# Optimization experiments

Hardware: AMD Instinct MI355X
Metric: run time of the kernel (lower is better)

The kernel has to match this reference:

```python
import jax, jax.numpy as jnp
import numpy as np

T, HID, H, KV, D = 2048, 2048, 16, 8, 128
EPS = 1e-6
THETA = 10000.0


def setup_inputs() -> dict:
    key = jax.random.key(0)
    ks = jax.random.split(key, 4)
    return {
        "positions": jnp.arange(T, dtype=jnp.int32),
        "hidden_states": jax.random.normal(ks[0], (T, HID), dtype=jnp.float32),
        "layernorm_weight": jnp.ones((HID,), dtype=jnp.float32),
        "qkv_weight": jax.random.normal(ks[1], ((H + 2 * KV) * D, HID), dtype=jnp.float32) * 0.02,
        "q_norm_weight": jnp.ones((D,), dtype=jnp.float32),
        "k_norm_weight": jnp.ones((D,), dtype=jnp.float32),
        "o_weight": jax.random.normal(ks[2], (HID, H * D), dtype=jnp.float32) * 0.02,
    }


def _rms(x, w, eps=EPS):
    var = jnp.mean(jnp.square(x), axis=-1, keepdims=True)
    return x * jax.lax.rsqrt(var + eps) * w


def _rope(x, pos):
    # NeoX-style rotary over full head_dim. x: [T, nH, D]
    inv_freq = 1.0 / (THETA ** (jnp.arange(0, D, 2, dtype=jnp.float32) / D))
    ang = pos.astype(jnp.float32)[:, None] * inv_freq  # [T, D/2]
    cos, sin = jnp.cos(ang)[:, None, :], jnp.sin(ang)[:, None, :]
    x1, x2 = x[..., : D // 2], x[..., D // 2 :]
    return jnp.concatenate([x1 * cos - x2 * sin, x2 * cos + x1 * sin], axis=-1)


def reference(positions, hidden_states, layernorm_weight, qkv_weight,
              q_norm_weight, k_norm_weight, o_weight):
    # Fused RMSNorm + QKV projection
    normed = _rms(hidden_states, layernorm_weight)                 # [T, HID]
    qkv = normed @ qkv_weight.T                                    # [T, (H+2KV)*D]
    q, k, v = jnp.split(qkv, [H * D, (H + KV) * D], axis=-1)
    q = _rms(q.reshape(T, H, D), q_norm_weight)                    # per-head q norm
    k = _rms(k.reshape(T, KV, D), k_norm_weight)                   # per-head k norm
    v = v.reshape(T, KV, D)
    # RoPE
    q = _rope(q, positions)
    k = _rope(k, positions)
    # GQA causal attention
    scale = D ** -0.5
    kr = jnp.repeat(k, H // KV, axis=1)                            # [T, H, D]
    vr = jnp.repeat(v, H // KV, axis=1)
    scores = jnp.einsum("qhd,khd->hqk", q, kr) * scale             # [H, T, T]
    mask = jnp.tril(jnp.ones((T, T), dtype=bool))
    scores = jnp.where(mask[None], scores, jnp.finfo(scores.dtype).min)
    attn = jax.nn.softmax(scores, axis=-1)
    out = jnp.einsum("hqk,khd->qhd", attn, vr).reshape(T, H * D)
    return out @ o_weight.T                                        # [T, HID]
```

## Files before the change

### kernel.cpp

```cpp
#include <hip/hip_runtime.h>
#include <cstdint>
#include <cstddef>

typedef __bf16 bf16;
typedef __attribute__((ext_vector_type(8))) __bf16 bf16x8;
typedef __attribute__((ext_vector_type(4))) __bf16 bf16x4v;
typedef __attribute__((ext_vector_type(4))) float f32x4;
typedef __attribute__((ext_vector_type(16))) float f32x16;
typedef __attribute__((ext_vector_type(4))) short short4v;

#define T_N   2048
#define HID_N 2048
#define NH    16
#define NKV   8
#define HD    128

#define MFMA(a, b, c)   __builtin_amdgcn_mfma_f32_16x16x32_bf16((a), (b), (c), 0, 0, 0)
#define MFMA32(a, b, c) __builtin_amdgcn_mfma_f32_32x32x16_bf16((a), (b), (c), 0, 0, 0)

__device__ __forceinline__ f32x4 MFMA16(short4v a, short4v b, f32x4 c) {
#if __has_builtin(__builtin_amdgcn_mfma_f32_16x16x16bf16_1k)
    return __builtin_amdgcn_mfma_f32_16x16x16bf16_1k(a, b, c, 0, 0, 0);
#else
    asm volatile("v_mfma_f32_16x16x16_bf16 %0, %1, %2, %0\n\ts_nop 7\n\ts_nop 7"
                 : "+v"(c) : "v"(a), "v"(b));
    return c;
#endif
}

__device__ __forceinline__ void gl_lds16(const void* g, void* l) {
    __builtin_amdgcn_global_load_lds(
        (const __attribute__((address_space(1))) unsigned int*)g,
        (__attribute__((address_space(3))) unsigned int*)l,
        16, 0, 0);
}

__device__ __forceinline__ uint32_t pk2(float a, float b) {
    union { bf16 h; unsigned short u; } ca, cb;
    ca.h = (bf16)a; cb.h = (bf16)b;
    return ((uint32_t)cb.u << 16) | ca.u;
}

__device__ __forceinline__ void y2cq(int y, int& ci, int& qt) {
    if (y < 25)       { ci = 0; qt = y + 7; }
    else if (y < 42)  { ci = 1; qt = y - 10; }
    else if (y < 51)  { ci = 2; qt = y - 19; }
    else if (y == 51) { ci = 3; qt = 31; }
    else { int z = y - 52; int k = 7 - (z >> 2); ci = z & 3; qt = 8 * ci + k - 1; }
}
__device__ __forceinline__ int yof(int ci, int qt) {
    int k = qt + 1 - 8 * ci;
    if (k >= 8) {
        if (ci == 0) return qt - 7;
        if (ci == 1) return qt + 10;
        if (ci == 2) return qt + 19;
        return 51;
    }
    return 52 + (7 - k) * 4 + ci;
}

__global__ __launch_bounds__(256) void k_pre(const float* __restrict__ qkvw,
                                             bf16* __restrict__ qkvw_b,
                                             const float* __restrict__ ow,
                                             bf16* __restrict__ ow_b,
                                             const float* __restrict__ hid,
                                             const float* __restrict__ lw,
                                             bf16* __restrict__ normed) {
    const int blk = blockIdx.x, tid = threadIdx.x;
    if (blk < 6144) {
        const float* src; bf16* dst;
        if (blk < 4096) { int i = blk * 2048 + tid * 8; src = qkvw + i; dst = qkvw_b + i; }
        else            { int i = (blk - 4096) * 2048 + tid * 8; src = ow + i; dst = ow_b + i; }
        float4 x = ((const float4*)src)[0], y = ((const float4*)src)[1];
        bf16x8 v;
        v[0] = (bf16)x.x; v[1] = (bf16)x.y; v[2] = (bf16)x.z; v[3] = (bf16)x.w;
        v[4] = (bf16)y.x; v[5] = (bf16)y.y; v[6] = (bf16)y.z; v[7] = (bf16)y.w;
        *(bf16x8*)dst = v;
        return;
    }
    const int row = blk - 6144;
    const float* xr = hid + (size_t)row * HID_N;
    float4 a = ((const float4*)xr)[tid * 2];
    float4 b = ((const float4*)xr)[tid * 2 + 1];
    float ss = a.x*a.x + a.y*a.y + a.z*a.z + a.w*a.w
             + b.x*b.x + b.y*b.y + b.z*b.z + b.w*b.w;
    #pragma unroll
    for (int m = 32; m; m >>= 1) ss += __shfl_xor(ss, m);
    __shared__ float red[4];
    if ((tid & 63) == 0) red[tid >> 6] = ss;
    __syncthreads();
    float tot = red[0] + red[1] + red[2] + red[3];
    float rs = rsqrtf(tot * (1.0f / HID_N) + 1e-6f);
    const float4* wr = (const float4*)(lw + tid * 8);
    float4 wa = wr[0], wb = wr[1];
    bf16x8 v;
    v[0] = (bf16)(a.x * rs * wa.x); v[1] = (bf16)(a.y * rs * wa.y);
    v[2] = (bf16)(a.z * rs * wa.z); v[3] = (bf16)(a.w * rs * wa.w);
    v[4] = (bf16)(b.x * rs * wb.x); v[5] = (bf16)(b.y * rs * wb.y);
    v[6] = (bf16)(b.z * rs * wb.z); v[7] = (bf16)(b.w * rs * wb.w);
    *(bf16x8*)(normed + (size_t)row * HID_N + tid * 8) = v;
}

__global__ __launch_bounds__(256, 3) void k_gemm_qkv(const bf16* __restrict__ A,
                                                     const bf16* __restrict__ B,
                                                     bf16* __restrict__ qkv3,
                                                     bf16* __restrict__ vb) {
    const int K = HID_N;
    __shared__ __attribute__((aligned(16))) bf16 As[128 * 64];
    __shared__ __attribute__((aligned(16))) bf16 Bs[128 * 64];
    const int tid = threadIdx.x;
    const int lane = tid & 63, wid = tid >> 6;
    const int wm = wid >> 1, wn = wid & 1;
    const int col31 = lane & 31, khalf = lane >> 5;
    const int orig = blockIdx.y * gridDim.x + blockIdx.x;
    const int wgid = (orig & 7) * 64 + (orig >> 3);
    const size_t bm = (size_t)(wgid >> 5) * 128, bn = (size_t)(wgid & 31) * 128;

    f32x16 acc[2][2] = {};
    const int srow = tid >> 3;
    const int schk = tid & 7;

    for (int k0 = 0; k0 < K; k0 += 64) {
        __syncthreads();
        #pragma unroll
        for (int c = 0; c < 4; c++) {
            int row = c * 32 + srow;
            int ka = (schk ^ (row & 7)) << 3;
            gl_lds16(A + (bm + row) * (size_t)K + k0 + ka,
                     (char*)As + c * 4096 + tid * 16);
            gl_lds16(B + (bn + row) * (size_t)K + k0 + ka,
                     (char*)Bs + c * 4096 + tid * 16);
        }
        __syncthreads();
        #pragma unroll
        for (int kb = 0; kb < 4; kb++) {
            bf16x8 af[2], bfr[2];
            #pragma unroll
            for (int mt = 0; mt < 2; mt++) {
                int row = wm * 64 + mt * 32 + col31;
                af[mt] = *(const bf16x8*)(As + row * 64 + (((2 * kb + khalf) ^ (row & 7)) << 3));
            }
            #pragma unroll
            for (int nt = 0; nt < 2; nt++) {
                int row = wn * 64 + nt * 32 + col31;
                bfr[nt] = *(const bf16x8*)(Bs + row * 64 + (((2 * kb + khalf) ^ (row & 7)) << 3));
            }
            #pragma unroll
            for (int mt = 0; mt < 2; mt++)
                #pragma unroll
                for (int nt = 0; nt < 2; nt++)
                    acc[mt][nt] = MFMA32(af[mt], bfr[nt], acc[mt][nt]);
        }
    }
    #pragma unroll
    for (int mt = 0; mt < 2; mt++)
        #pragma unroll
        for (int nt = 0; nt < 2; nt++)
            #pragma unroll
            for (int i = 0; i < 16; i++) {
                int rowl = (i & 3) + 8 * (i >> 2) + 4 * khalf;
                size_t row = bm + wm * 64 + mt * 32 + rowl;
                size_t col = bn + wn * 64 + nt * 32 + col31;
                bf16 val = (bf16)acc[mt][nt][i];
                if (col < 3072) qkv3[row * 3072 + col] = val;
                else            vb[row * 1024 + (col - 3072)] = val;
            }
}

__global__ __launch_bounds__(256, 3) void k_gemm_bt64(const bf16* __restrict__ A,
                                                      const bf16* __restrict__ B,
                                                      float* __restrict__ C,
                                                      int M, int N, int K) {
    __shared__ __attribute__((aligned(16))) bf16 As[64 * 64];
    __shared__ __attribute__((aligned(16))) bf16 Bs[128 * 64];
    const int tid = threadIdx.x;
    const int lane = tid & 63, wid = tid >> 6;
    const int col31 = lane & 31, khalf = lane >> 5;
    const int orig = blockIdx.y * gridDim.x + blockIdx.x;
    const int wgid = (orig & 7) * 64 + (orig >> 3);
    const size_t bm = (size_t)(wgid >> 4) * 64, bn = (size_t)(wgid & 15) * 128;

    f32x16 acc[2] = {};
    const int srow = tid >> 3;
    const int schk = tid & 7;

    for (int k0 = 0; k0 < K; k0 += 64) {
        __syncthreads();
        #pragma unroll
        for (int c = 0; c < 2; c++) {
            int row = c * 32 + srow;
            int ka = (schk ^ (row & 7)) << 3;
            gl_lds16(A + (bm + row) * (size_t)K + k0 + ka,
                     (char*)As + c * 4096 + tid * 16);
        }
        #pragma unroll
        for (int c = 0; c < 4; c++) {
            int row = c * 32 + srow;
            int ka = (schk ^ (row & 7)) << 3;
            gl_lds16(B + (bn + row) * (size_t)K + k0 + ka,
                     (char*)Bs + c * 4096 + tid * 16);
        }
        __syncthreads();
        #pragma unroll
        for (int kb = 0; kb < 4; kb++) {
            bf16x8 af[2], bfr;
            #pragma unroll
            for (int mt = 0; mt < 2; mt++) {
                int row = mt * 32 + col31;
                af[mt] = *(const bf16x8*)(As + row * 64 + (((2 * kb + khalf) ^ (row & 7)) << 3));
            }
            {
                int row = wid * 32 + col31;
                bfr = *(const bf16x8*)(Bs + row * 64 + (((2 * kb + khalf) ^ (row & 7)) << 3));
            }
            #pragma unroll
            for (int mt = 0; mt < 2; mt++)
                acc[mt] = MFMA32(af[mt], bfr, acc[mt]);
        }
    }
    #pragma unroll
    for (int mt = 0; mt < 2; mt++)
        #pragma unroll
        for (int i = 0; i < 16; i++) {
            int rowl = (i & 3) + 8 * (i >> 2) + 4 * khalf;
            size_t row = bm + mt * 32 + rowl;
            size_t col = bn + wid * 32 + col31;
            C[row * (size_t)N + col] = acc[mt][i];
        }
}

__global__ __launch_bounds__(256) void k_mid(const bf16* __restrict__ qkv3,
                                             const float* __restrict__ qw,
                                             const float* __restrict__ kw,
                                             const int* __restrict__ pos,
                                             bf16* __restrict__ q,
                                             bf16* __restrict__ k,
                                             const bf16* __restrict__ vin,
                                             bf16* __restrict__ vT) {
    const int tid = threadIdx.x;
    if (blockIdx.y == 12) {
        const int bx = blockIdx.x;
        if (bx >= 512) return;
        __shared__ bf16 tile[64][72];
        const int tb = bx & 31, db = bx >> 5;
        const int row = tid >> 2, cc = tid & 3;
        const bf16* src = vin + (size_t)(tb * 64 + row) * 1024 + db * 64 + cc * 16;
        bf16x8 a = *(const bf16x8*)(src);
        bf16x8 b = *(const bf16x8*)(src + 8);
        #pragma unroll
        for (int i = 0; i < 8; i++) tile[row][cc * 16 + i] = a[i];
        #pragma unroll
        for (int i = 0; i < 8; i++) tile[row][cc * 16 + 8 + i] = b[i];
        __syncthreads();
        bf16* dst = vT + (size_t)(db * 64 + row) * 2048 + tb * 64 + cc * 16;
        bf16x8 o1, o2;
        #pragma unroll
        for (int i = 0; i < 8; i++) o1[i] = tile[cc * 16 + i][row];
        #pragma unroll
        for (int i = 0; i < 8; i++) o2[i] = tile[cc * 16 + 8 + i][row];
        *(bf16x8*)dst = o1;
        *(bf16x8*)(dst + 8) = o2;
        return;
    }
    const int t = blockIdx.x;
    const int half = tid >> 7, d = tid & 127;
    const int slot = blockIdx.y * 2 + half;
    const bool isq = slot < 16;
    const int h = isq ? slot : slot - 16;
    float x = (float)qkv3[(size_t)t * 3072 + slot * 128 + d];
    float ss = x * x;
    #pragma unroll
    for (int m = 32; m; m >>= 1) ss += __shfl_xor(ss, m);
    __shared__ float red[4];
    __shared__ float sh[256];
    if ((tid & 63) == 0) red[tid >> 6] = ss;
    __syncthreads();
    float rs = rsqrtf((red[half * 2] + red[half * 2 + 1]) * (1.0f / HD) + 1e-6f);
    float nx = x * rs * (isq ? qw[d] : kw[d]);
    sh[tid] = nx;
    __syncthreads();
    float other = sh[tid ^ 64];
    int j = d & 63;
    float ang = (float)pos[t] * __powf(10000.f, -(float)j * (1.f / 64.f));
    float s, c;
    __sincosf(ang, &s, &c);
    float o = (d < 64) ? (nx * c - other * s) : (nx * c + other * s);
    bf16* dst = isq ? (q + ((size_t)t * NH + h) * HD + d)
                    : (k + ((size_t)t * NKV + h) * HD + d);
    *dst = (bf16)o;
}

__global__ __launch_bounds__(256, 3) void k_flash(const bf16* __restrict__ Q,
                                                  const bf16* __restrict__ K,
                                                  const bf16* __restrict__ VT,
                                                  bf16* __restrict__ On,
                                                  float* __restrict__ ml) {
    __shared__ __attribute__((aligned(16))) bf16 Ks2[2][64 * 128];
    __shared__ __attribute__((aligned(16))) bf16 Vt[128 * 64];

    const int tid = threadIdx.x, lane = tid & 63, w = tid >> 6;
    const int r = lane & 15, g = lane >> 4;
    const int h = blockIdx.x, y = blockIdx.y;
    int ci, qt;
    y2cq(y, ci, qt);
    const int c0 = ci * 8;
    const int ntl = min(qt + 1 - c0, 8);
    const int q0 = qt * 64;
    const int gh = h >> 1;
    const int q0w = q0 + w * 16;

    const int rowk = tid >> 4, posc = tid & 15;
    const int vrow = tid >> 3, vkb = tid & 7;
    const bf16* VTh = VT + (size_t)gh * 128 * 2048;

    bf16x8 qf[4];
    #pragma unroll
    for (int ks = 0; ks < 4; ks++)
        qf[ks] = *(const bf16x8*)(Q + ((size_t)(q0w + r) * NH + h) * HD + ks * 32 + g * 8);

    f32x4 acc[8] = {};
    float m_run = -1e30f, l_run = 0.f;
    const float scale = 0.08838834764831845f;

    {
        const int kv0 = c0 * 64;
        #pragma unroll
        for (int c = 0; c < 4; c++) {
            int row = c * 16 + rowk;
            int srcc = posc ^ (row & 7);
            gl_lds16(K + ((size_t)(kv0 + row) * NKV + gh) * HD + srcc * 8,
                     (char*)&Ks2[0][0] + c * 4096 + tid * 16);
        }
        asm volatile("s_waitcnt vmcnt(0)" ::: "memory");
        __builtin_amdgcn_s_barrier();
    }

    for (int t = 0; t < ntl; ++t) {
        const int b = t & 1;
        const int kv0 = (c0 + t) * 64;
        const bool pf = (t + 1 < ntl);
        #pragma unroll
        for (int it = 0; it < 4; it++) {
            int d = it * 32 + vrow;
            int srck = (vkb ^ (vrow & 7)) * 8;
            gl_lds16(VTh + (size_t)d * 2048 + kv0 + srck,
                     (char*)&Vt[0] + it * 4096 + tid * 16);
        }
        if (pf) {
            const int kv1 = kv0 + 64;
            #pragma unroll
            for (int c = 0; c < 4; c++) {
                int row = c * 16 + rowk;
                int srcc = posc ^ (row & 7);
                gl_lds16(K + ((size_t)(kv1 + row) * NKV + gh) * HD + srcc * 8,
                         (char*)&Ks2[0][0] + (b ^ 1) * 16384 + c * 4096 + tid * 16);
            }
        }
        const bool compute = (kv0 <= q0w + 15);
        union PB { uint32_t u[2]; short4v s; };
        PB pbu[4];
        if (compute) {
            const bf16* Kb = &Ks2[b][0];
            const bool fullt = (kv0 + 63 <= q0w);
            float sc[4][4];
            __builtin_amdgcn_s_setprio(1);
            #pragma unroll
            for (int t4 = 0; t4 < 4; t4++) {
                f32x4 S = {};
                #pragma unroll
                for (int ks = 0; ks < 4; ks++) {
                    int row = t4 * 16 + r;
                    bf16x8 kf = *(const bf16x8*)(Kb + row * 128 + (((4 * ks + g) ^ (row & 7)) * 8));
                    S = MFMA(kf, qf[ks], S);
                }
                if (fullt) {
                    #pragma unroll
                    for (int j = 0; j < 4; j++) sc[t4][j] = S[j] * scale;
                } else {
                    #pragma unroll
                    for (int j = 0; j < 4; j++) {
                        int kg = kv0 + t4 * 16 + 4 * g + j;
                        sc[t4][j] = (kg <= q0w + r) ? S[j] * scale : -1e30f;
                    }
                }
            }
            __builtin_amdgcn_s_setprio(0);
            float mx = sc[0][0];
            #pragma unroll
            for (int t4 = 0; t4 < 4; t4++)
                #pragma unroll
                for (int j = 0; j < 4; j++) mx = fmaxf(mx, sc[t4][j]);
            mx = fmaxf(mx, __shfl_xor(mx, 16));
            mx = fmaxf(mx, __shfl_xor(mx, 32));
            const bool nr = __all(mx <= m_run + 8.0f) != 0;
            float mn, alpha;
            if (nr) { mn = m_run; alpha = 1.0f; }
            else    { mn = fmaxf(m_run, mx); alpha = __expf(m_run - mn); m_run = mn; }
            float rsum = 0.f;
            #pragma unroll
            for (int t4 = 0; t4 < 4; t4++)
                #pragma unroll
                for (int j = 0; j < 4; j++) {
                    sc[t4][j] = __expf(sc[t4][j] - mn);
                    rsum += sc[t4][j];
                }
            rsum += __shfl_xor(rsum, 16);
            rsum += __shfl_xor(rsum, 32);
            l_run = l_run * alpha + rsum;
            if (!nr) {
                #pragma unroll
                for (int f = 0; f < 8; f++)
                    #pragma unroll
                    for (int j = 0; j < 4; j++) acc[f][j] *= alpha;
            }
            #pragma unroll
            for (int t4 = 0; t4 < 4; t4++) {
                pbu[t4].u[0] = pk2(sc[t4][0], sc[t4][1]);
                pbu[t4].u[1] = pk2(sc[t4][2], sc[t4][3]);
            }
        }
        if (pf) asm volatile("s_waitcnt vmcnt(4)" ::: "memory");
        else    asm volatile("s_waitcnt vmcnt(0)" ::: "memory");
        __builtin_amdgcn_s_barrier();
        if (compute) {
            const char* Vb = (const char*)&Vt[0];
            __builtin_amdgcn_s_setprio(1);
            #pragma unroll
            for (int f = 0; f < 8; f++) {
                #pragma unroll
                for (int t4 = 0; t4 < 4; t4++) {
                    short4v vf = *(const short4v*)(Vb + f * 2048 + r * 128 +
                                  (((2 * t4 + (g >> 1)) ^ (r & 7)) * 16) + (g & 1) * 8);
                    acc[f] = MFMA16(vf, pbu[t4].s, acc[f]);
                }
            }
            __builtin_amdgcn_s_setprio(0);
        }
        asm volatile("s_waitcnt vmcnt(0)" ::: "memory");
        __builtin_amdgcn_s_barrier();
    }
    const int lr = w * 16 + r;
    float inv_l = 1.0f / l_run;
    bf16* Ob = On + ((size_t)(h * 80 + y)) * 8192 + lr * 128;
    #pragma unroll
    for (int f = 0; f < 8; f++) {
        bf16x4v ov;
        #pragma unroll
        for (int j = 0; j < 4; j++) ov[j] = (bf16)(acc[f][j] * inv_l);
        *(bf16x4v*)(Ob + f * 16 + 4 * g) = ov;
    }
    if (g == 0) {
        float* mlp = ml + ((size_t)(h * 80 + y)) * 128;
        mlp[lr] = m_run;
        mlp[64 + lr] = l_run;
    }
}

__global__ __launch_bounds__(256) void k_comb(const bf16* __restrict__ On,
                                              const float* __restrict__ ml,
                                              bf16* __restrict__ ao) {
    const int h = blockIdx.x, qt = blockIdx.y;
    const int tid = threadIdx.x;
    const int dc = tid & 15;
    const int qr = tid >> 4;
    const int nc = 1 + (qt >= 8) + (qt >= 16) + (qt >= 24);
    int ys[4];
    #pragma unroll
    for (int i = 0; i < 4; i++) ys[i] = (i < nc) ? yof(i, qt) : 0;
    #pragma unroll
    for (int p = 0; p < 4; p++) {
        const int lq = p * 16 + qr;
        float mi[4], li[4], wi[4];
        float mstar = -1e30f;
        for (int i = 0; i < 4; i++) {
            if (i < nc) {
                const float* pml = ml + ((size_t)(h * 80 + ys[i])) * 128;
                mi[i] = pml[lq]; li[i] = pml[64 + lq];
                mstar = fmaxf(mstar, mi[i]);
            }
        }
        float wsum = 0.f;
        for (int i = 0; i < 4; i++) {
            if (i < nc) { wi[i] = li[i] * __expf(mi[i] - mstar); wsum += wi[i]; }
            else wi[i] = 0.f;
        }
        float inv = 1.f / wsum;
        float o[8] = {};
        for (int i = 0; i < 4; i++) {
            if (i < nc) {
                bf16x8 v = *(const bf16x8*)(On + ((size_t)(h * 80 + ys[i])) * 8192 +
                                            lq * 128 + dc * 8);
                float wn = wi[i] * inv;
                #pragma unroll
                for (int j = 0; j < 8; j++) o[j] += wn * (float)v[j];
            }
        }
        bf16x8 ov;
        #pragma unroll
        for (int j = 0; j < 8; j++) ov[j] = (bf16)o[j];
        const int q = qt * 64 + lq;
        *(bf16x8*)(ao + ((size_t)q * NH + h) * HD + dc * 8) = ov;
    }
}

extern "C" void kernel_launch(void* const* d_in, const int* in_sizes, int n_in,
                              void* d_out, int out_size, void* d_ws, size_t ws_size,
                              hipStream_t stream) {
    const int*   pos  = (const int*)d_in[0];
    const float* hid  = (const float*)d_in[1];
    const float* lw   = (const float*)d_in[2];
    const float* qkvw = (const float*)d_in[3];
    const float* qnw  = (const float*)d_in[4];
    const float* knw  = (const float*)d_in[5];
    const float* ow   = (const float*)d_in[6];
    float* out = (float*)d_out;

    char* ws = (char*)d_ws;
    bf16*  qkvw_b = (bf16*)(ws);
    bf16*  ow_b   = (bf16*)(ws + (16u << 20));
    bf16*  normed = (bf16*)(ws + (24u << 20));
    bf16*  qkv3   = (bf16*)(ws + (32u << 20));
    bf16*  qb     = (bf16*)(ws + (64u << 20));
    bf16*  kb     = (bf16*)(ws + (72u << 20));
    bf16*  vb     = (bf16*)(ws + (76u << 20));
    bf16*  ao     = normed;
    bf16*  On     = (bf16*)(ws + (32u << 20));
    float* ml     = (float*)(ws + (54u << 20));
    bf16*  vT     = (bf16*)(ws + (56u << 20));

    k_pre<<<8192, 256, 0, stream>>>(qkvw, qkvw_b, ow, ow_b, hid, lw, normed);
    k_gemm_qkv<<<dim3(32, 16), 256, 0, stream>>>(normed, qkvw_b, qkv3, vb);
    k_mid<<<dim3(T_N, 13), 256, 0, stream>>>(qkv3, qnw, knw, pos, qb, kb, vb, vT);
    k_flash<<<dim3(NH, 80), 256, 0, stream>>>(qb, kb, vT, On, ml);
    k_comb<<<dim3(NH, 32), 256, 0, stream>>>(On, ml, ao);
    k_gemm_bt64<<<dim3(16, 32), 256, 0, stream>>>(ao, ow_b, out, 2048, 2048, 2048);
}
```

Baseline: 177.0 us.

## Fuse q/k RMSNorm+RoPE into QKV GEMM epilogue; double-buffer output GEMM

The per-head q/k RMSNorm and rotary embedding move into the QKV GEMM epilogue. Accumulators are staged through swizzled shared memory, each row is normalized and rotated, and q/k are written directly, so the qkv3 intermediate and the separate k_mid pass are gone. The V transpose becomes its own small kernel. Separately, the output-projection GEMM gets double-buffered LDS with prefetch of the next K tile and setprio around the MFMAs, so loads overlap compute. The cost is a heavier epilogue in the QKV GEMM and twice the LDS in the output GEMM, which may reduce occupancy.

```diff
diff --git a/kernel.cpp b/kernel.cpp
--- a/kernel.cpp
+++ b/kernel.cpp
@@ -103,7 +103,11 @@
 
 __global__ __launch_bounds__(256, 3) void k_gemm_qkv(const bf16* __restrict__ A,
                                                      const bf16* __restrict__ B,
-                                                     bf16* __restrict__ qkv3,
+                                                     const float* __restrict__ qw,
+                                                     const float* __restrict__ kw,
+                                                     const int* __restrict__ pos,
+                                                     bf16* __restrict__ qb,
+                                                     bf16* __restrict__ kb,
                                                      bf16* __restrict__ vb) {
     const int K = HID_N;
     __shared__ __attribute__((aligned(16))) bf16 As[128 * 64];
@@ -133,17 +137,17 @@
         }
         __syncthreads();
         #pragma unroll
-        for (int kb = 0; kb < 4; kb++) {
+        for (int kb2 = 0; kb2 < 4; kb2++) {
             bf16x8 af[2], bfr[2];
             #pragma unroll
             for (int mt = 0; mt < 2; mt++) {
                 int row = wm * 64 + mt * 32 + col31;
-                af[mt] = *(const bf16x8*)(As + row * 64 + (((2 * kb + khalf) ^ (row & 7)) << 3));
+                af[mt] = *(const bf16x8*)(As + row * 64 + (((2 * kb2 + khalf) ^ (row & 7)) << 3));
             }
             #pragma unroll
             for (int nt = 0; nt < 2; nt++) {
                 int row = wn * 64 + nt * 32 + col31;
-                bfr[nt] = *(const bf16x8*)(Bs + row * 64 + (((2 * kb + khalf) ^ (row & 7)) << 3));
+                bfr[nt] = *(const bf16x8*)(Bs + row * 64 + (((2 * kb2 + khalf) ^ (row & 7)) << 3));
             }
             #pragma unroll
             for (int mt = 0; mt < 2; mt++)
@@ -152,27 +156,88 @@
                     acc[mt][nt] = MFMA32(af[mt], bfr[nt], acc[mt][nt]);
         }
     }
-    #pragma unroll
-    for (int mt = 0; mt < 2; mt++)
-        #pragma unroll
-        for (int nt = 0; nt < 2; nt++)
-            #pragma unroll
-            for (int i = 0; i < 16; i++) {
-                int rowl = (i & 3) + 8 * (i >> 2) + 4 * khalf;
-                size_t row = bm + wm * 64 + mt * 32 + rowl;
-                size_t col = bn + wn * 64 + nt * 32 + col31;
-                bf16 val = (bf16)acc[mt][nt][i];
-                if (col < 3072) qkv3[row * 3072 + col] = val;
-                else            vb[row * 1024 + (col - 3072)] = val;
-            }
+
+    const int nb = wgid & 31;
+    if (nb >= 24) {
+        #pragma unroll
+        for (int mt = 0; mt < 2; mt++)
+            #pragma unroll
+            for (int nt = 0; nt < 2; nt++)
+                #pragma unroll
+                for (int i = 0; i < 16; i++) {
+                    int rowl = (i & 3) + 8 * (i >> 2) + 4 * khalf;
+                    size_t row = bm + wm * 64 + mt * 32 + rowl;
+                    int col = (nb - 24) * 128 + wn * 64 + nt * 32 + col31;
+                    vb[row * 1024 + col] = (bf16)acc[mt][nt][i];
+                }
+        return;
+    }
+    const bool isq = nb < 16;
+    const int hh = isq ? nb : nb - 16;
+    const float* nw = isq ? qw : kw;
+    float* Cs = (float*)As;
+    const int lrow = tid >> 2, qc = tid & 3;
+    const int sw = (lrow & 7) << 2;
+    #pragma unroll
+    for (int half = 0; half < 2; half++) {
+        __syncthreads();
+        if (wm == half) {
+            #pragma unroll
+            for (int mt = 0; mt < 2; mt++)
+                #pragma unroll
+                for (int nt = 0; nt < 2; nt++)
+                    #pragma unroll
+                    for (int i = 0; i < 16; i++) {
+                        int rl = mt * 32 + (i & 3) + 8 * (i >> 2) + 4 * khalf;
+                        int lc = wn * 64 + nt * 32 + col31;
+                        Cs[rl * 128 + (lc ^ ((rl & 7) << 2))] = acc[mt][nt][i];
+                    }
+        }
+        __syncthreads();
+        float ssq = 0.f;
+        #pragma unroll
+        for (int j4 = 0; j4 < 8; j4++) {
+            f32x4 v = *(const f32x4*)(Cs + lrow * 128 + ((qc * 32 + j4 * 4) ^ sw));
+            ssq += v[0]*v[0] + v[1]*v[1] + v[2]*v[2] + v[3]*v[3];
+        }
+        ssq += __shfl_xor(ssq, 1);
+        ssq += __shfl_xor(ssq, 2);
+        float rs = rsqrtf(ssq * (1.0f / 128.f) + 1e-6f);
+        const int grow = (int)bm + half * 64 + lrow;
+        const float pt = (float)pos[grow];
+        bf16 outv[32];
+        #pragma unroll
+        for (int j4 = 0; j4 < 8; j4++) {
+            int c0 = qc * 32 + j4 * 4;
+            f32x4 v  = *(const f32x4*)(Cs + lrow * 128 + (c0 ^ sw));
+            f32x4 vp = *(const f32x4*)(Cs + lrow * 128 + ((c0 ^ 64) ^ sw));
+            #pragma unroll
+            for (int e = 0; e < 4; e++) {
+                int c = c0 + e;
+                int jj = c & 63;
+                float ang = pt * __powf(10000.f, -(float)jj * (1.f / 64.f));
+                float sn, cn;
+                __sincosf(ang, &sn, &cn);
+                float nv  = v[e]  * rs * nw[c];
+                float nv2 = vp[e] * rs * nw[c ^ 64];
+                outv[j4 * 4 + e] = (bf16)((c < 64) ? (nv * cn - nv2 * sn)
+                                                   : (nv * cn + nv2 * sn));
+            }
+        }
+        bf16* dst = isq ? (qb + ((size_t)grow * NH + hh) * HD + qc * 32)
+                        : (kb + ((size_t)grow * NKV + hh) * HD + qc * 32);
+        #pragma unroll
+        for (int s = 0; s < 4; s++)
+            *(bf16x8*)(dst + s * 8) = *(bf16x8*)(outv + s * 8);
+    }
 }
 
 __global__ __launch_bounds__(256, 3) void k_gemm_bt64(const bf16* __restrict__ A,
                                                       const bf16* __restrict__ B,
                                                       float* __restrict__ C,
                                                       int M, int N, int K) {
-    __shared__ __attribute__((aligned(16))) bf16 As[64 * 64];
-    __shared__ __attribute__((aligned(16))) bf16 Bs[128 * 64];
+    __shared__ __attribute__((aligned(16))) bf16 As[2][64 * 64];
+    __shared__ __attribute__((aligned(16))) bf16 Bs[2][128 * 64];
     const int tid = threadIdx.x;
     const int lane = tid & 63, wid = tid >> 6;
     const int col31 = lane & 31, khalf = lane >> 5;
@@ -184,39 +249,62 @@
     const int srow = tid >> 3;
     const int schk = tid & 7;
 
+    #pragma unroll
+    for (int c = 0; c < 2; c++) {
+        int row = c * 32 + srow;
+        int ka = (schk ^ (row & 7)) << 3;
+        gl_lds16(A + (bm + row) * (size_t)K + ka, (char*)&As[0][0] + c * 4096 + tid * 16);
+    }
+    #pragma unroll
+    for (int c = 0; c < 4; c++) {
+        int row = c * 32 + srow;
+        int ka = (schk ^ (row & 7)) << 3;
+        gl_lds16(B + (bn + row) * (size_t)K + ka, (char*)&Bs[0][0] + c * 4096 + tid * 16);
+    }
+    asm volatile("s_waitcnt vmcnt(0) lgkmcnt(0)" ::: "memory");
+    __builtin_amdgcn_s_barrier();
+
     for (int k0 = 0; k0 < K; k0 += 64) {
-        __syncthreads();
-        #pragma unroll
-        for (int c = 0; c < 2; c++) {
-            int row = c * 32 + srow;
-            int ka = (schk ^ (row & 7)) << 3;
-            gl_lds16(A + (bm + row) * (size_t)K + k0 + ka,
-                     (char*)As + c * 4096 + tid * 16);
-        }
-        #pragma unroll
-        for (int c = 0; c < 4; c++) {
-            int row = c * 32 + srow;
-            int ka = (schk ^ (row & 7)) << 3;
-            gl_lds16(B + (bn + row) * (size_t)K + k0 + ka,
-                     (char*)Bs + c * 4096 + tid * 16);
-        }
-        __syncthreads();
-        #pragma unroll
-        for (int kb = 0; kb < 4; kb++) {
+        const int cur = (k0 >> 6) & 1;
+        if (k0 + 64 < K) {
+            const int kn = k0 + 64;
+            #pragma unroll
+            for (int c = 0; c < 2; c++) {
+                int row = c * 32 + srow;
+                int ka = (schk ^ (row & 7)) << 3;
+                gl_lds16(A + (bm + row) * (size_t)K + kn + ka,
+                         (char*)&As[cur ^ 1][0] + c * 4096 + tid * 16);
+            }
+            #pragma unroll
+            for (int c = 0; c < 4; c++) {
+                int row = c * 32 + srow;
+                int ka = (schk ^ (row & 7)) << 3;
+                gl_lds16(B + (bn + row) * (size_t)K + kn + ka,
+                         (char*)&Bs[cur ^ 1][0] + c * 4096 + tid * 16);
+            }
+        }
+        const bf16* Ab = &As[cur][0];
+        const bf16* Bb = &Bs[cur][0];
+        __builtin_amdgcn_s_setprio(1);
+        #pragma unroll
+        for (int kb2 = 0; kb2 < 4; kb2++) {
             bf16x8 af[2], bfr;
             #pragma unroll
             for (int mt = 0; mt < 2; mt++) {
                 int row = mt * 32 + col31;
-                af[mt] = *(const bf16x8*)(As + row * 64 + (((2 * kb + khalf) ^ (row & 7)) << 3));
+                af[mt] = *(const bf16x8*)(Ab + row * 64 + (((2 * kb2 + khalf) ^ (row & 7)) << 3));
             }
             {
                 int row = wid * 32 + col31;
-                bfr = *(const bf16x8*)(Bs + row * 64 + (((2 * kb + khalf) ^ (row & 7)) << 3));
+                bfr = *(const bf16x8*)(Bb + row * 64 + (((2 * kb2 + khalf) ^ (row & 7)) << 3));
             }
             #pragma unroll
             for (int mt = 0; mt < 2; mt++)
                 acc[mt] = MFMA32(af[mt], bfr, acc[mt]);
         }
+        __builtin_amdgcn_s_setprio(0);
+        asm volatile("s_waitcnt vmcnt(0) lgkmcnt(0)" ::: "memory");
+        __builtin_amdgcn_s_barrier();
     }
     #pragma unroll
     for (int mt = 0; mt < 2; mt++)
@@ -229,65 +317,29 @@
         }
 }
 
-__global__ __launch_bounds__(256) void k_mid(const bf16* __restrict__ qkv3,
-                                             const float* __restrict__ qw,
-                                             const float* __restrict__ kw,
-                                             const int* __restrict__ pos,
-                                             bf16* __restrict__ q,
-                                             bf16* __restrict__ k,
-                                             const bf16* __restrict__ vin,
-                                             bf16* __restrict__ vT) {
+__global__ __launch_bounds__(256) void k_vt(const bf16* __restrict__ in,
+                                            bf16* __restrict__ outp) {
+    __shared__ bf16 tile[64][72];
+    const int tb = blockIdx.x;
+    const int db = blockIdx.y;
     const int tid = threadIdx.x;
-    if (blockIdx.y == 12) {
-        const int bx = blockIdx.x;
-        if (bx >= 512) return;
-        __shared__ bf16 tile[64][72];
-        const int tb = bx & 31, db = bx >> 5;
-        const int row = tid >> 2, cc = tid & 3;
-        const bf16* src = vin + (size_t)(tb * 64 + row) * 1024 + db * 64 + cc * 16;
-        bf16x8 a = *(const bf16x8*)(src);
-        bf16x8 b = *(const bf16x8*)(src + 8);
-        #pragma unroll
-        for (int i = 0; i < 8; i++) tile[row][cc * 16 + i] = a[i];
-        #pragma unroll
-        for (int i = 0; i < 8; i++) tile[row][cc * 16 + 8 + i] = b[i];
-        __syncthreads();
-        bf16* dst = vT + (size_t)(db * 64 + row) * 2048 + tb * 64 + cc * 16;
-        bf16x8 o1, o2;
-        #pragma unroll
-        for (int i = 0; i < 8; i++) o1[i] = tile[cc * 16 + i][row];
-        #pragma unroll
-        for (int i = 0; i < 8; i++) o2[i] = tile[cc * 16 + 8 + i][row];
-        *(bf16x8*)dst = o1;
-        *(bf16x8*)(dst + 8) = o2;
-        return;
-    }
-    const int t = blockIdx.x;
-    const int half = tid >> 7, d = tid & 127;
-    const int slot = blockIdx.y * 2 + half;
-    const bool isq = slot < 16;
-    const int h = isq ? slot : slot - 16;
-    float x = (float)qkv3[(size_t)t * 3072 + slot * 128 + d];
-    float ss = x * x;
-    #pragma unroll
-    for (int m = 32; m; m >>= 1) ss += __shfl_xor(ss, m);
-    __shared__ float red[4];
-    __shared__ float sh[256];
-    if ((tid & 63) == 0) red[tid >> 6] = ss;
+    const int row = tid >> 2, cc = tid & 3;
+    const bf16* src = in + (size_t)(tb * 64 + row) * 1024 + db * 64 + cc * 16;
+    bf16x8 a = *(const bf16x8*)(src);
+    bf16x8 b = *(const bf16x8*)(src + 8);
+    #pragma unroll
+    for (int i = 0; i < 8; i++) tile[row][cc * 16 + i] = a[i];
+    #pragma unroll
+    for (int i = 0; i < 8; i++) tile[row][cc * 16 + 8 + i] = b[i];
     __syncthreads();
-    float rs = rsqrtf((red[half * 2] + red[half * 2 + 1]) * (1.0f / HD) + 1e-6f);
-    float nx = x * rs * (isq ? qw[d] : kw[d]);
-    sh[tid] = nx;
-    __syncthreads();
-    float other = sh[tid ^ 64];
-    int j = d & 63;
-    float ang = (float)pos[t] * __powf(10000.f, -(float)j * (1.f / 64.f));
-    float s, c;
-    __sincosf(ang, &s, &c);
-    float o = (d < 64) ? (nx * c - other * s) : (nx * c + other * s);
-    bf16* dst = isq ? (q + ((size_t)t * NH + h) * HD + d)
-                    : (k + ((size_t)t * NKV + h) * HD + d);
-    *dst = (bf16)o;
+    bf16* dst = outp + (size_t)(db * 64 + row) * 2048 + tb * 64 + cc * 16;
+    bf16x8 o1, o2;
+    #pragma unroll
+    for (int i = 0; i < 8; i++) o1[i] = tile[cc * 16 + i][row];
+    #pragma unroll
+    for (int i = 0; i < 8; i++) o2[i] = tile[cc * 16 + 8 + i][row];
+    *(bf16x8*)dst = o1;
+    *(bf16x8*)(dst + 8) = o2;
 }
 
 __global__ __launch_bounds__(256, 3) void k_flash(const bf16* __restrict__ Q,
@@ -519,7 +571,6 @@
     bf16*  qkvw_b = (bf16*)(ws);
     bf16*  ow_b   = (bf16*)(ws + (16u << 20));
     bf16*  normed = (bf16*)(ws + (24u << 20));
-    bf16*  qkv3   = (bf16*)(ws + (32u << 20));
     bf16*  qb     = (bf16*)(ws + (64u << 20));
     bf16*  kb     = (bf16*)(ws + (72u << 20));
     bf16*  vb     = (bf16*)(ws + (76u << 20));
@@ -529,8 +580,8 @@
     bf16*  vT     = (bf16*)(ws + (56u << 20));
 
     k_pre<<<8192, 256, 0, stream>>>(qkvw, qkvw_b, ow, ow_b, hid, lw, normed);
-    k_gemm_qkv<<<dim3(32, 16), 256, 0, stream>>>(normed, qkvw_b, qkv3, vb);
-    k_mid<<<dim3(T_N, 13), 256, 0, stream>>>(qkv3, qnw, knw, pos, qb, kb, vb, vT);
+    k_gemm_qkv<<<dim3(32, 16), 256, 0, stream>>>(normed, qkvw_b, qnw, knw, pos, qb, kb, vb);
+    k_vt<<<dim3(32, 16), 256, 0, stream>>>(vb, vT);
     k_flash<<<dim3(NH, 80), 256, 0, stream>>>(qb, kb, vT, On, ml);
     k_comb<<<dim3(NH, 32), 256, 0, stream>>>(On, ml, ao);
     k_gemm_bt64<<<dim3(16, 32), 256, 0, stream>>>(ao, ow_b, out, 2048, 2048, 2048);
```

New measurement: 185.7 us. +4.9%, slower.

## Double-buffer LDS in both GEMMs and shrink QKV tile to 64x128

Applied to the files above, without the earlier changes.

Both bf16 GEMMs now use two LDS buffers, so the global-to-LDS loads for the next K step are issued before computing on the current one, with one barrier per iteration instead of two. The QKV GEMM moves from 128x128 to 64x128 tiles, doubling the grid to 1024 blocks, and both GEMMs get a new block-to-tile mapping and a raised wave priority around the MFMA section. The aim is to hide global load latency and improve CU occupancy. The cost is more LDS per block and less data reuse per tile in the QKV GEMM.

```diff
diff --git a/kernel.cpp b/kernel.cpp
--- a/kernel.cpp
+++ b/kernel.cpp
@@ -101,122 +101,167 @@
     *(bf16x8*)(normed + (size_t)row * HID_N + tid * 8) = v;
 }
 
-__global__ __launch_bounds__(256, 3) void k_gemm_qkv(const bf16* __restrict__ A,
-                                                     const bf16* __restrict__ B,
-                                                     bf16* __restrict__ qkv3,
-                                                     bf16* __restrict__ vb) {
+__global__ __launch_bounds__(256, 3) void k_gemm_qkv64(const bf16* __restrict__ A,
+                                                       const bf16* __restrict__ B,
+                                                       bf16* __restrict__ qkv3,
+                                                       bf16* __restrict__ vb) {
     const int K = HID_N;
-    __shared__ __attribute__((aligned(16))) bf16 As[128 * 64];
-    __shared__ __attribute__((aligned(16))) bf16 Bs[128 * 64];
+    __shared__ __attribute__((aligned(16))) bf16 As[2][64 * 64];
+    __shared__ __attribute__((aligned(16))) bf16 Bs[2][128 * 64];
     const int tid = threadIdx.x;
     const int lane = tid & 63, wid = tid >> 6;
-    const int wm = wid >> 1, wn = wid & 1;
     const int col31 = lane & 31, khalf = lane >> 5;
     const int orig = blockIdx.y * gridDim.x + blockIdx.x;
-    const int wgid = (orig & 7) * 64 + (orig >> 3);
-    const size_t bm = (size_t)(wgid >> 5) * 128, bn = (size_t)(wgid & 31) * 128;
-
-    f32x16 acc[2][2] = {};
+    const int wgid = (orig & 7) * 128 + (orig >> 3);
+    const size_t bm = (size_t)(wgid & 31) * 64, bn = (size_t)(wgid >> 5) * 128;
+
+    f32x16 acc[2] = {};
     const int srow = tid >> 3;
     const int schk = tid & 7;
 
+    #pragma unroll
+    for (int c = 0; c < 2; c++) {
+        int row = c * 32 + srow;
+        int ka = (schk ^ (row & 7)) << 3;
+        gl_lds16(A + (bm + row) * (size_t)K + ka, (char*)&As[0][0] + c * 4096 + tid * 16);
+    }
+    #pragma unroll
+    for (int c = 0; c < 4; c++) {
+        int row = c * 32 + srow;
+        int ka = (schk ^ (row & 7)) << 3;
+        gl_lds16(B + (bn + row) * (size_t)K + ka, (char*)&Bs[0][0] + c * 4096 + tid * 16);
+    }
+    asm volatile("s_waitcnt vmcnt(0) lgkmcnt(0)" ::: "memory");
+    __builtin_amdgcn_s_barrier();
+
     for (int k0 = 0; k0 < K; k0 += 64) {
-        __syncthreads();
-        #pragma unroll
-        for (int c = 0; c < 4; c++) {
-            int row = c * 32 + srow;
-            int ka = (schk ^ (row & 7)) << 3;
-            gl_lds16(A + (bm + row) * (size_t)K + k0 + ka,
-                     (char*)As + c * 4096 + tid * 16);
-            gl_lds16(B + (bn + row) * (size_t)K + k0 + ka,
-                     (char*)Bs + c * 4096 + tid * 16);
-        }
-        __syncthreads();
-        #pragma unroll
-        for (int kb = 0; kb < 4; kb++) {
-            bf16x8 af[2], bfr[2];
+        const int cur = (k0 >> 6) & 1;
+        if (k0 + 64 < K) {
+            const int kn = k0 + 64;
+            #pragma unroll
+            for (int c = 0; c < 2; c++) {
+                int row = c * 32 + srow;
+                int ka = (schk ^ (row & 7)) << 3;
+                gl_lds16(A + (bm + row) * (size_t)K + kn + ka,
+                         (char*)&As[cur ^ 1][0] + c * 4096 + tid * 16);
+            }
+            #pragma unroll
+            for (int c = 0; c < 4; c++) {
+                int row = c * 32 + srow;
+                int ka = (schk ^ (row & 7)) << 3;
+                gl_lds16(B + (bn + row) * (size_t)K + kn + ka,
+                         (char*)&Bs[cur ^ 1][0] + c * 4096 + tid * 16);
+            }
+        }
+        const bf16* Ab = &As[cur][0];
+        const bf16* Bb = &Bs[cur][0];
+        __builtin_amdgcn_s_setprio(1);
+        #pragma unroll
+        for (int kb2 = 0; kb2 < 4; kb2++) {
+            bf16x8 af[2], bfr;
             #pragma unroll
             for (int mt = 0; mt < 2; mt++) {
-                int row = wm * 64 + mt * 32 + col31;
-                af[mt] = *(const bf16x8*)(As + row * 64 + (((2 * kb + khalf) ^ (row & 7)) << 3));
-            }
-            #pragma unroll
-            for (int nt = 0; nt < 2; nt++) {
-                int row = wn * 64 + nt * 32 + col31;
-                bfr[nt] = *(const bf16x8*)(Bs + row * 64 + (((2 * kb + khalf) ^ (row & 7)) << 3));
+                int row = mt * 32 + col31;
+                af[mt] = *(const bf16x8*)(Ab + row * 64 + (((2 * kb2 + khalf) ^ (row & 7)) << 3));
+            }
+            {
+                int row = wid * 32 + col31;
+                bfr = *(const bf16x8*)(Bb + row * 64 + (((2 * kb2 + khalf) ^ (row & 7)) << 3));
             }
             #pragma unroll
             for (int mt = 0; mt < 2; mt++)
-                #pragma unroll
-                for (int nt = 0; nt < 2; nt++)
-                    acc[mt][nt] = MFMA32(af[mt], bfr[nt], acc[mt][nt]);
-        }
+                acc[mt] = MFMA32(af[mt], bfr, acc[mt]);
+        }
+        __builtin_amdgcn_s_setprio(0);
+        asm volatile("s_waitcnt vmcnt(0) lgkmcnt(0)" ::: "memory");
+        __builtin_amdgcn_s_barrier();
     }
     #pragma unroll
     for (int mt = 0; mt < 2; mt++)
         #pragma unroll
-        for (int nt = 0; nt < 2; nt++)
-            #pragma unroll
-            for (int i = 0; i < 16; i++) {
-                int rowl = (i & 3) + 8 * (i >> 2) + 4 * khalf;
-                size_t row = bm + wm * 64 + mt * 32 + rowl;
-                size_t col = bn + wn * 64 + nt * 32 + col31;
-                bf16 val = (bf16)acc[mt][nt][i];
-                if (col < 3072) qkv3[row * 3072 + col] = val;
-                else            vb[row * 1024 + (col - 3072)] = val;
-            }
+        for (int i = 0; i < 16; i++) {
+            int rowl = (i & 3) + 8 * (i >> 2) + 4 * khalf;
+            size_t row = bm + mt * 32 + rowl;
+            size_t col = bn + wid * 32 + col31;
+            bf16 val = (bf16)acc[mt][i];
+            if (col < 3072) qkv3[row * 3072 + col] = val;
+            else            vb[row * 1024 + (col - 3072)] = val;
+        }
 }
 
 __global__ __launch_bounds__(256, 3) void k_gemm_bt64(const bf16* __restrict__ A,
                                                       const bf16* __restrict__ B,
                                                       float* __restrict__ C,
                                                       int M, int N, int K) {
-    __shared__ __attribute__((aligned(16))) bf16 As[64 * 64];
-    __shared__ __attribute__((aligned(16))) bf16 Bs[128 * 64];
+    __shared__ __attribute__((aligned(16))) bf16 As[2][64 * 64];
+    __shared__ __attribute__((aligned(16))) bf16 Bs[2][128 * 64];
     const int tid = threadIdx.x;
     const int lane = tid & 63, wid = tid >> 6;
     const int col31 = lane & 31, khalf = lane >> 5;
     const int orig = blockIdx.y * gridDim.x + blockIdx.x;
     const int wgid = (orig & 7) * 64 + (orig >> 3);
-    const size_t bm = (size_t)(wgid >> 4) * 64, bn = (size_t)(wgid & 15) * 128;
+    const size_t bm = (size_t)(wgid & 31) * 64, bn = (size_t)(wgid >> 5) * 128;
 
     f32x16 acc[2] = {};
     const int srow = tid >> 3;
     const int schk = tid & 7;
 
+    #pragma unroll
+    for (int c = 0; c < 2; c++) {
+        int row = c * 32 + srow;
+        int ka = (schk ^ (row & 7)) << 3;
+        gl_lds16(A + (bm + row) * (size_t)K + ka, (char*)&As[0][0] + c * 4096 + tid * 16);
+    }
+    #pragma unroll
+    for (int c = 0; c < 4; c++) {
+        int row = c * 32 + srow;
+        int ka = (schk ^ (row & 7)) << 3;
+        gl_lds16(B + (bn + row) * (size_t)K + ka, (char*)&Bs[0][0] + c * 4096 + tid * 16);
+    }
+    asm volatile("s_waitcnt vmcnt(0) lgkmcnt(0)" ::: "memory");
+    __builtin_amdgcn_s_barrier();
+
     for (int k0 = 0; k0 < K; k0 += 64) {
-        __syncthreads();
-        #pragma unroll
-        for (int c = 0; c < 2; c++) {
-            int row = c * 32 + srow;
-            int ka = (schk ^ (row & 7)) << 3;
-            gl_lds16(A + (bm + row) * (size_t)K + k0 + ka,
-                     (char*)As + c * 4096 + tid * 16);
-        }
-        #pragma unroll
-        for (int c = 0; c < 4; c++) {
-            int row = c * 32 + srow;
-            int ka = (schk ^ (row & 7)) << 3;
-            gl_lds16(B + (bn + row) * (size_t)K + k0 + ka,
-                     (char*)Bs + c * 4096 + tid * 16);
-        }
-        __syncthreads();
-        #pragma unroll
-        for (int kb = 0; kb < 4; kb++) {
+        const int cur = (k0 >> 6) & 1;
+        if (k0 + 64 < K) {
+            const int kn = k0 + 64;
+            #pragma unroll
+            for (int c = 0; c < 2; c++) {
+                int row = c * 32 + srow;
+                int ka = (schk ^ (row & 7)) << 3;
+                gl_lds16(A + (bm + row) * (size_t)K + kn + ka,
+                         (char*)&As[cur ^ 1][0] + c * 4096 + tid * 16);
+            }
+            #pragma unroll
+            for (int c = 0; c < 4; c++) {
+                int row = c * 32 + srow;
+                int ka = (schk ^ (row & 7)) << 3;
+                gl_lds16(B + (bn + row) * (size_t)K + kn + ka,
+                         (char*)&Bs[cur ^ 1][0] + c * 4096 + tid * 16);
+            }
+        }
+        const bf16* Ab = &As[cur][0];
+        const bf16* Bb = &Bs[cur][0];
+        __builtin_amdgcn_s_setprio(1);
+        #pragma unroll
+        for (int kb2 = 0; kb2 < 4; kb2++) {
             bf16x8 af[2], bfr;
             #pragma unroll
             for (int mt = 0; mt < 2; mt++) {
                 int row = mt * 32 + col31;
-                af[mt] = *(const bf16x8*)(As + row * 64 + (((2 * kb + khalf) ^ (row & 7)) << 3));
+                af[mt] = *(const bf16x8*)(Ab + row * 64 + (((2 * kb2 + khalf) ^ (row & 7)) << 3));
             }
             {
                 int row = wid * 32 + col31;
-                bfr = *(const bf16x8*)(Bs + row * 64 + (((2 * kb + khalf) ^ (row & 7)) << 3));
+                bfr = *(const bf16x8*)(Bb + row * 64 + (((2 * kb2 + khalf) ^ (row & 7)) << 3));
             }
             #pragma unroll
             for (int mt = 0; mt < 2; mt++)
                 acc[mt] = MFMA32(af[mt], bfr, acc[mt]);
         }
+        __builtin_amdgcn_s_setprio(0);
+        asm volatile("s_waitcnt vmcnt(0) lgkmcnt(0)" ::: "memory");
+        __builtin_amdgcn_s_barrier();
     }
     #pragma unroll
     for (int mt = 0; mt < 2; mt++)
@@ -529,7 +574,7 @@
     bf16*  vT     = (bf16*)(ws + (56u << 20));
 
     k_pre<<<8192, 256, 0, stream>>>(qkvw, qkvw_b, ow, ow_b, hid, lw, normed);
-    k_gemm_qkv<<<dim3(32, 16), 256, 0, stream>>>(normed, qkvw_b, qkv3, vb);
+    k_gemm_qkv64<<<dim3(32, 32), 256, 0, stream>>>(normed, qkvw_b, qkv3, vb);
     k_mid<<<dim3(T_N, 13), 256, 0, stream>>>(qkv3, qnw, knw, pos, qb, kb, vb, vT);
     k_flash<<<dim3(NH, 80), 256, 0, stream>>>(qb, kb, vT, On, ml);
     k_comb<<<dim3(NH, 32), 256, 0, stream>>>(On, ml, ao);
```

Measured after the change: 192.5 us. 8.7% more time.
